# Kernel optimization log

Hardware: AMD Instinct MI355X
Metric: run time of the kernel (lower is better)

Reference implementation:

```python
import jax, jax.numpy as jnp
import numpy as np

NUM_HEADS = 8


def setup_inputs() -> dict:
    key = jax.random.key(0)
    k1, k2, k3 = jax.random.split(key, 3)
    B, L, E, H = 4, 2048, 256, NUM_HEADS
    x = jax.random.normal(k1, (B, L, E), dtype=jnp.float32)
    W_qkv = jax.random.normal(k2, (E, H * E * 3), dtype=jnp.float32) * 0.02
    W_out = jax.random.normal(k3, (H * E, E), dtype=jnp.float32) * 0.02
    return {"x": x, "W_qkv": W_qkv, "W_out": W_out}


def reference(x, W_qkv, W_out):
    B, L, E = x.shape
    H = NUM_HEADS
    qkv = x @ W_qkv  # [B, L, 3*H*E]
    q, k, v = jnp.split(qkv, 3, axis=-1)  # each [B, L, H*E]
    # reshape(B, L, H, E) then move heads before sequence -> [B, H, L, E]
    q = q.reshape(B, L, H, E).transpose(0, 2, 1, 3)
    k = k.reshape(B, L, H, E).transpose(0, 2, 1, 3)
    v = v.reshape(B, L, H, E).transpose(0, 2, 1, 3)
    scale = 1.0 / jnp.sqrt(jnp.asarray(E, dtype=x.dtype))
    scores = jnp.einsum("bhqe,bhke->bhqk", q, k) * scale  # [B, H, L, L]
    attn = jax.nn.softmax(scores, axis=-1)
    out = jnp.einsum("bhqk,bhke->bhqe", attn, v)  # [B, H, L, E]
    out = out.transpose(0, 2, 1, 3).reshape(B, L, H * E)
    return out @ W_out  # [B, L, E]
```

## Files before the change

### kernel.cpp

```cpp
#include <hip/hip_runtime.h>
#include <cstdint>
#include <cstddef>

typedef __bf16 bf16_t;
typedef __bf16 bf16x8 __attribute__((ext_vector_type(8)));
typedef __bf16 bf16x4 __attribute__((ext_vector_type(4)));
typedef float  f32x4  __attribute__((ext_vector_type(4)));
typedef float  f32x16 __attribute__((ext_vector_type(16)));

#define MFMA16(a, b, c) __builtin_amdgcn_mfma_f32_16x16x32_bf16((a), (b), (c), 0, 0, 0)
#define MFMA32(a, b, c) __builtin_amdgcn_mfma_f32_32x32x16_bf16((a), (b), (c), 0, 0, 0)
#define CVTPK(d, a, b) \
  asm("v_cvt_pk_bf16_f32 %0, %1, %2" : "=v"(d) : "v"(a), "v"(b))
#define PLSWAP(a, b) \
  asm("v_permlane32_swap_b32 %0, %1" : "+v"(a), "+v"(b))

__device__ __forceinline__ void gload_lds16(const bf16_t* g, bf16_t* l) {
  __builtin_amdgcn_global_load_lds(
      (__attribute__((address_space(1))) void*)((void*)g),
      (__attribute__((address_space(3))) void*)l, 16, 0, 0);
}

__global__ __launch_bounds__(256) void cvt_f32_bf16(
    const float* __restrict__ in, bf16_t* __restrict__ out, int n) {
  const int i = (blockIdx.x * 256 + threadIdx.x) * 4;
  if (i + 3 < n) {
    const float4 v = *(const float4*)(in + i);
    bf16x4 o;
    o[0] = (bf16_t)v.x; o[1] = (bf16_t)v.y; o[2] = (bf16_t)v.z; o[3] = (bf16_t)v.w;
    *(bf16x4*)(out + i) = o;
  }
}

__global__ __launch_bounds__(256) void transpose_f32_bf16(
    const float* __restrict__ in, bf16_t* __restrict__ out, int R, int C) {
  __shared__ bf16_t tile[32][33];
  const int bc = blockIdx.x * 32, br = blockIdx.y * 32;
  const int tx = threadIdx.x, ty = threadIdx.y;
#pragma unroll
  for (int i = 0; i < 32; i += 8)
    tile[ty + i][tx] = (bf16_t)in[(size_t)(br + ty + i) * C + bc + tx];
  __syncthreads();
#pragma unroll
  for (int i = 0; i < 32; i += 8)
    out[(size_t)(bc + ty + i) * R + br + tx] = tile[tx][ty + i];
}

template <int EPI>
__global__ __launch_bounds__(256) void gemm_bt(
    const bf16_t* __restrict__ A, const bf16_t* __restrict__ Bt,
    void* __restrict__ Cout, bf16_t* __restrict__ Vt, int M, int N, int K) {
  __shared__ __align__(16) bf16_t As[128 * 32];
  __shared__ __align__(16) bf16_t Bs[128 * 32];
  const int tid = threadIdx.x;
  const int lane = tid & 63, w = tid >> 6;
  const int wm = w >> 1, wn = w & 1;
  const int bm = blockIdx.y * 128, bn = blockIdx.x * 128;
  const int l15 = lane & 15, l4 = lane >> 4;

  f32x4 acc[4][4] = {};

  for (int k0 = 0; k0 < K; k0 += 32) {
    __syncthreads();
#pragma unroll
    for (int i = 0; i < 2; ++i) {
      const int idx = i * 256 + tid;
      const int r = idx >> 2, s = idx & 3;
      const int ss = s ^ (r & 3);
      gload_lds16(A + (size_t)(bm + r) * K + k0 + ss * 8, &As[idx * 8]);
      gload_lds16(Bt + (size_t)(bn + r) * K + k0 + ss * 8, &Bs[idx * 8]);
    }
    __syncthreads();
    bf16x8 af[4], bfr[4];
#pragma unroll
    for (int f = 0; f < 4; ++f) {
      const int ra = wm * 64 + f * 16 + l15;
      const int rb = wn * 64 + f * 16 + l15;
      af[f]  = *(const bf16x8*)&As[ra * 32 + (l4 ^ (ra & 3)) * 8];
      bfr[f] = *(const bf16x8*)&Bs[rb * 32 + (l4 ^ (rb & 3)) * 8];
    }
#pragma unroll
    for (int i = 0; i < 4; ++i)
#pragma unroll
      for (int j = 0; j < 4; ++j) acc[i][j] = MFMA16(af[i], bfr[j], acc[i][j]);
  }

#pragma unroll
  for (int i = 0; i < 4; ++i) {
    const int gr = bm + wm * 64 + i * 16 + l4 * 4;
#pragma unroll
    for (int j = 0; j < 4; ++j) {
      const int gc = bn + wn * 64 + j * 16 + l15;
      if constexpr (EPI == 0) {
        float* C = (float*)Cout;
#pragma unroll
        for (int r = 0; r < 4; ++r)
          C[(size_t)(gr + r) * N + gc] = acc[i][j][r];
      } else {
        bf16_t* C = (bf16_t*)Cout;
        if (gc < 2048) {
#pragma unroll
          for (int r = 0; r < 4; ++r)
            C[(size_t)(gr + r) * 4096 + gc] = (bf16_t)(acc[i][j][r] * 0.0625f);
        } else if (gc < 4096) {
#pragma unroll
          for (int r = 0; r < 4; ++r)
            C[(size_t)(gr + r) * 4096 + gc] = (bf16_t)acc[i][j][r];
        } else {
          const int c = gc - 4096, h = c >> 8, d = c & 255;
          const int b = gr >> 11, lt = gr & 2047;
          bf16x4 pk;
#pragma unroll
          for (int r = 0; r < 4; ++r) pk[r] = (bf16_t)acc[i][j][r];
          *(bf16x4*)&Vt[((size_t)(b * 8 + h) * 256 + d) * 2048 + lt] = pk;
        }
      }
    }
  }
}

__global__ __launch_bounds__(256, 2) void attn_fwd(
    const bf16_t* __restrict__ qk, const bf16_t* __restrict__ vt,
    bf16_t* __restrict__ ao) {
  __shared__ __align__(16) bf16_t Ks[2][32 * 256];
  __shared__ __align__(16) bf16_t Vs[2][256 * 32];
  const int tid = threadIdx.x, lane = tid & 63, w = tid >> 6;
  const int l31 = lane & 31, h5 = lane >> 5;
  const int p4 = l31 & 15, pv2 = (l31 >> 1) & 3;
  const int bid = blockIdx.x;
  const int swz = (bid & 7) * 64 + (bid >> 3);
  const int qt = swz & 15;
  const int bh = swz >> 4;
  const int bb = bh >> 3, hh = bh & 7;

  const int qcol = qt * 128 + w * 32 + l31;
  const bf16_t* qbase =
      qk + (size_t)(bb * 2048 + qcol) * 4096 + hh * 256 + h5 * 8;
  bf16x8 qf[16];
#pragma unroll
  for (int s = 0; s < 16; ++s) qf[s] = *(const bf16x8*)(qbase + s * 16);

  const bf16_t* kg = qk + (size_t)(bb * 2048) * 4096 + 2048 + hh * 256;
  const bf16_t* vg = vt + (size_t)bh * 256 * 2048;

#define STAGE_TILES(bufidx, tile)                                           \
  {                                                                         \
    const int t32 = (tile) * 32;                                            \
    _Pragma("unroll") for (int c = 0; c < 4; ++c) {                         \
      const int idx = c * 256 + tid;                                        \
      const int kr = idx >> 5, kse = idx & 31;                              \
      gload_lds16(kg + (size_t)(t32 + kr) * 4096 + ((kse ^ (kr & 15)) * 8), \
                  &Ks[bufidx][idx * 8]);                                    \
    }                                                                       \
    _Pragma("unroll") for (int c = 0; c < 4; ++c) {                         \
      const int idx = c * 256 + tid;                                        \
      const int vr = idx >> 2, vse = idx & 3;                               \
      gload_lds16(vg + (size_t)vr * 2048 + t32 +                            \
                      ((vse ^ ((vr >> 1) & 3)) * 8),                        \
                  &Vs[bufidx][idx * 8]);                                    \
    }                                                                       \
  }

  STAGE_TILES(0, 0);
  STAGE_TILES(1, 1);

  f32x16 o[8] = {};
  float m = -1e30f, lsum = 0.f;

  for (int kv = 0; kv < 64; ++kv) {
    const int cur = kv & 1;
    asm volatile("s_waitcnt vmcnt(8)" ::: "memory");
    __builtin_amdgcn_s_barrier();
    __builtin_amdgcn_sched_barrier(0);
    const bf16_t* Kc = Ks[cur];
    const bf16_t* Vc = Vs[cur];

    f32x16 sa = {};
    __builtin_amdgcn_s_setprio(1);
#pragma unroll
    for (int s = 0; s < 16; ++s) {
      bf16x8 kf = *(const bf16x8*)
          ((const char*)Kc + l31 * 512 + (((2 * s + h5) ^ p4) << 4));
      sa = MFMA32(kf, qf[s], sa);
    }
    __builtin_amdgcn_s_setprio(0);

    float pm = sa[0];
#pragma unroll
    for (int r = 1; r < 16; ++r) pm = fmaxf(pm, sa[r]);
    pm = fmaxf(pm, __shfl_xor(pm, 32));
    if (!__all(pm <= m + 8.0f)) {
      const float mn = fmaxf(m, pm);
      const float al = __expf(m - mn);
      m = mn;
      lsum *= al;
#pragma unroll
      for (int dt = 0; dt < 8; ++dt)
#pragma unroll
        for (int r = 0; r < 16; ++r) o[dt][r] *= al;
    }
    float rs = 0.f;
#pragma unroll
    for (int r = 0; r < 16; ++r) { sa[r] = __expf(sa[r] - m); rs += sa[r]; }
    rs += __shfl_xor(rs, 32);
    lsum += rs;

    __builtin_amdgcn_s_setprio(1);
#define PV_KSTEP(SA, c0, s2)                                                \
    {                                                                       \
      unsigned w0, w1, w2, w3;                                              \
      CVTPK(w0, SA[4 * (c0) + 0], SA[4 * (c0) + 1]);                        \
      CVTPK(w2, SA[4 * (c0) + 4], SA[4 * (c0) + 5]);                        \
      PLSWAP(w0, w2);                                                       \
      CVTPK(w1, SA[4 * (c0) + 2], SA[4 * (c0) + 3]);                        \
      CVTPK(w3, SA[4 * (c0) + 6], SA[4 * (c0) + 7]);                        \
      PLSWAP(w1, w3);                                                       \
      union { unsigned u[4]; bf16x8 v; } pu;                                \
      pu.u[0] = w0; pu.u[1] = w1; pu.u[2] = w2; pu.u[3] = w3;               \
      _Pragma("unroll") for (int dt = 0; dt < 8; ++dt) {                    \
        bf16x8 vf = *(const bf16x8*)((const char*)Vc +                      \
            (dt * 32 + l31) * 64 + ((((s2) * 2 + h5) ^ pv2) << 4));         \
        o[dt] = MFMA32(vf, pu.v, o[dt]);                                    \
      }                                                                     \
    }
    PV_KSTEP(sa, 0, 0);
    PV_KSTEP(sa, 2, 1);
    __builtin_amdgcn_s_setprio(0);

    __builtin_amdgcn_sched_barrier(0);
    __builtin_amdgcn_s_barrier();
    __builtin_amdgcn_sched_barrier(0);
    STAGE_TILES(cur, (kv + 2) & 63);
  }

  const float inv = 1.0f / lsum;
  bf16_t* aor = ao + (size_t)(bb * 2048 + qcol) * 2048 + hh * 256 + 4 * h5;
#pragma unroll
  for (int dt = 0; dt < 8; ++dt)
#pragma unroll
    for (int c = 0; c < 4; ++c) {
      bf16x4 ov;
#pragma unroll
      for (int bq = 0; bq < 4; ++bq) ov[bq] = (bf16_t)(o[dt][4 * c + bq] * inv);
      *(bf16x4*)(aor + dt * 32 + 8 * c) = ov;
    }
}

extern "C" void kernel_launch(void* const* d_in, const int* in_sizes, int n_in,
                              void* d_out, int out_size, void* d_ws,
                              size_t ws_size, hipStream_t stream) {
  (void)in_sizes; (void)n_in; (void)out_size; (void)ws_size;
  const float* x    = (const float*)d_in[0];
  const float* wqkv = (const float*)d_in[1];
  const float* wout = (const float*)d_in[2];
  float* out = (float*)d_out;

  char* ws = (char*)d_ws;
  bf16_t* xb  = (bf16_t*)(ws);
  bf16_t* wqt = (bf16_t*)(ws + 4194304);
  bf16_t* wot = (bf16_t*)(ws + 7340032);
  bf16_t* qkb = (bf16_t*)(ws + 8388608);
  bf16_t* vtb = (bf16_t*)(ws + 8388608 + 67108864);
  bf16_t* aob = (bf16_t*)(ws + 8388608 + 67108864 + 33554432);

  cvt_f32_bf16<<<2048, 256, 0, stream>>>(x, xb, 8192 * 256);
  transpose_f32_bf16<<<dim3(192, 8), dim3(32, 8), 0, stream>>>(wqkv, wqt, 256, 6144);
  transpose_f32_bf16<<<dim3(8, 64), dim3(32, 8), 0, stream>>>(wout, wot, 2048, 256);
  gemm_bt<1><<<dim3(48, 64), 256, 0, stream>>>(xb, wqt, qkb, vtb, 8192, 6144, 256);
  attn_fwd<<<512, 256, 0, stream>>>(qkb, vtb, aob);
  gemm_bt<0><<<dim3(2, 64), 256, 0, stream>>>(aob, wot, out, nullptr, 8192, 256, 2048);
}
```

Baseline: 331.3 us.

## Process two 32-row query sets per wave in attention to reuse K/V fragments

Each wave now computes attention for 64 query rows (two independent 32-row sets with separate softmax state), reusing each K and V LDS fragment for two MFMAs. The grid is halved and launch bounds drop to one block per CU to allow the doubled accumulator and Q register footprint. This reduces LDS reads and global K/V staging per query, at the cost of lower occupancy and possible register pressure or spills.

```diff
diff --git a/kernel.cpp b/kernel.cpp
--- a/kernel.cpp
+++ b/kernel.cpp
@@ -119,7 +119,7 @@
   }
 }
 
-__global__ __launch_bounds__(256, 2) void attn_fwd(
+__global__ __launch_bounds__(256, 1) void attn_fwd(
     const bf16_t* __restrict__ qk, const bf16_t* __restrict__ vt,
     bf16_t* __restrict__ ao) {
   __shared__ __align__(16) bf16_t Ks[2][32 * 256];
@@ -128,17 +128,20 @@
   const int l31 = lane & 31, h5 = lane >> 5;
   const int p4 = l31 & 15, pv2 = (l31 >> 1) & 3;
   const int bid = blockIdx.x;
-  const int swz = (bid & 7) * 64 + (bid >> 3);
-  const int qt = swz & 15;
-  const int bh = swz >> 4;
+  const int swz = (bid & 7) * 32 + (bid >> 3);
+  const int qt = swz & 7;
+  const int bh = swz >> 3;
   const int bb = bh >> 3, hh = bh & 7;
 
-  const int qcol = qt * 128 + w * 32 + l31;
-  const bf16_t* qbase =
-      qk + (size_t)(bb * 2048 + qcol) * 4096 + hh * 256 + h5 * 8;
-  bf16x8 qf[16];
-#pragma unroll
-  for (int s = 0; s < 16; ++s) qf[s] = *(const bf16x8*)(qbase + s * 16);
+  const int qcolA = qt * 256 + w * 64 + l31;
+  const bf16_t* qbaseA =
+      qk + (size_t)(bb * 2048 + qcolA) * 4096 + hh * 256 + h5 * 8;
+  bf16x8 qfA[16], qfB[16];
+#pragma unroll
+  for (int s = 0; s < 16; ++s) {
+    qfA[s] = *(const bf16x8*)(qbaseA + s * 16);
+    qfB[s] = *(const bf16x8*)(qbaseA + (size_t)32 * 4096 + s * 16);
+  }
 
   const bf16_t* kg = qk + (size_t)(bb * 2048) * 4096 + 2048 + hh * 256;
   const bf16_t* vg = vt + (size_t)bh * 256 * 2048;
@@ -164,8 +167,8 @@
   STAGE_TILES(0, 0);
   STAGE_TILES(1, 1);
 
-  f32x16 o[8] = {};
-  float m = -1e30f, lsum = 0.f;
+  f32x16 oA[8] = {}, oB[8] = {};
+  float mA = -1e30f, lsA = 0.f, mB = -1e30f, lsB = 0.f;
 
   for (int kv = 0; kv < 64; ++kv) {
     const int cur = kv & 1;
@@ -175,38 +178,41 @@
     const bf16_t* Kc = Ks[cur];
     const bf16_t* Vc = Vs[cur];
 
-    f32x16 sa = {};
+    f32x16 saA = {}, saB = {};
     __builtin_amdgcn_s_setprio(1);
 #pragma unroll
     for (int s = 0; s < 16; ++s) {
       bf16x8 kf = *(const bf16x8*)
           ((const char*)Kc + l31 * 512 + (((2 * s + h5) ^ p4) << 4));
-      sa = MFMA32(kf, qf[s], sa);
+      saA = MFMA32(kf, qfA[s], saA);
+      saB = MFMA32(kf, qfB[s], saB);
     }
     __builtin_amdgcn_s_setprio(0);
 
-    float pm = sa[0];
-#pragma unroll
-    for (int r = 1; r < 16; ++r) pm = fmaxf(pm, sa[r]);
-    pm = fmaxf(pm, __shfl_xor(pm, 32));
-    if (!__all(pm <= m + 8.0f)) {
-      const float mn = fmaxf(m, pm);
-      const float al = __expf(m - mn);
-      m = mn;
-      lsum *= al;
-#pragma unroll
-      for (int dt = 0; dt < 8; ++dt)
-#pragma unroll
-        for (int r = 0; r < 16; ++r) o[dt][r] *= al;
-    }
-    float rs = 0.f;
-#pragma unroll
-    for (int r = 0; r < 16; ++r) { sa[r] = __expf(sa[r] - m); rs += sa[r]; }
-    rs += __shfl_xor(rs, 32);
-    lsum += rs;
-
-    __builtin_amdgcn_s_setprio(1);
-#define PV_KSTEP(SA, c0, s2)                                                \
+#define SOFTMAX_SET(SA, M_, LS_, O_)                                        \
+    {                                                                       \
+      float pm = SA[0];                                                     \
+      _Pragma("unroll") for (int r = 1; r < 16; ++r) pm = fmaxf(pm, SA[r]); \
+      pm = fmaxf(pm, __shfl_xor(pm, 32));                                   \
+      if (!__all(pm <= M_ + 8.0f)) {                                        \
+        const float mn = fmaxf(M_, pm);                                     \
+        const float al = __expf(M_ - mn);                                   \
+        M_ = mn;                                                            \
+        LS_ *= al;                                                          \
+        _Pragma("unroll") for (int dt = 0; dt < 8; ++dt)                    \
+          _Pragma("unroll") for (int r = 0; r < 16; ++r) O_[dt][r] *= al;   \
+      }                                                                     \
+      float rs = 0.f;                                                       \
+      _Pragma("unroll") for (int r = 0; r < 16; ++r) {                      \
+        SA[r] = __expf(SA[r] - M_); rs += SA[r];                            \
+      }                                                                     \
+      rs += __shfl_xor(rs, 32);                                             \
+      LS_ += rs;                                                            \
+    }
+    SOFTMAX_SET(saA, mA, lsA, oA);
+    SOFTMAX_SET(saB, mB, lsB, oB);
+
+#define MAKE_PU(SA, c0, PU)                                                 \
     {                                                                       \
       unsigned w0, w1, w2, w3;                                              \
       CVTPK(w0, SA[4 * (c0) + 0], SA[4 * (c0) + 1]);                        \
@@ -215,16 +221,22 @@
       CVTPK(w1, SA[4 * (c0) + 2], SA[4 * (c0) + 3]);                        \
       CVTPK(w3, SA[4 * (c0) + 6], SA[4 * (c0) + 7]);                        \
       PLSWAP(w1, w3);                                                       \
-      union { unsigned u[4]; bf16x8 v; } pu;                                \
-      pu.u[0] = w0; pu.u[1] = w1; pu.u[2] = w2; pu.u[3] = w3;               \
-      _Pragma("unroll") for (int dt = 0; dt < 8; ++dt) {                    \
-        bf16x8 vf = *(const bf16x8*)((const char*)Vc +                      \
-            (dt * 32 + l31) * 64 + ((((s2) * 2 + h5) ^ pv2) << 4));         \
-        o[dt] = MFMA32(vf, pu.v, o[dt]);                                    \
-      }                                                                     \
-    }
-    PV_KSTEP(sa, 0, 0);
-    PV_KSTEP(sa, 2, 1);
+      PU.u[0] = w0; PU.u[1] = w1; PU.u[2] = w2; PU.u[3] = w3;               \
+    }
+    __builtin_amdgcn_s_setprio(1);
+#pragma unroll
+    for (int s2 = 0; s2 < 2; ++s2) {
+      union { unsigned u[4]; bf16x8 v; } puA, puB;
+      MAKE_PU(saA, 2 * s2, puA);
+      MAKE_PU(saB, 2 * s2, puB);
+#pragma unroll
+      for (int dt = 0; dt < 8; ++dt) {
+        bf16x8 vf = *(const bf16x8*)((const char*)Vc +
+            (dt * 32 + l31) * 64 + (((s2 * 2 + h5) ^ pv2) << 4));
+        oA[dt] = MFMA32(vf, puA.v, oA[dt]);
+        oB[dt] = MFMA32(vf, puB.v, oB[dt]);
+      }
+    }
     __builtin_amdgcn_s_setprio(0);
 
     __builtin_amdgcn_sched_barrier(0);
@@ -233,16 +245,21 @@
     STAGE_TILES(cur, (kv + 2) & 63);
   }
 
-  const float inv = 1.0f / lsum;
-  bf16_t* aor = ao + (size_t)(bb * 2048 + qcol) * 2048 + hh * 256 + 4 * h5;
+  const float invA = 1.0f / lsA, invB = 1.0f / lsB;
+  bf16_t* aorA = ao + (size_t)(bb * 2048 + qcolA) * 2048 + hh * 256 + 4 * h5;
+  bf16_t* aorB = aorA + (size_t)32 * 2048;
 #pragma unroll
   for (int dt = 0; dt < 8; ++dt)
 #pragma unroll
     for (int c = 0; c < 4; ++c) {
-      bf16x4 ov;
-#pragma unroll
-      for (int bq = 0; bq < 4; ++bq) ov[bq] = (bf16_t)(o[dt][4 * c + bq] * inv);
-      *(bf16x4*)(aor + dt * 32 + 8 * c) = ov;
+      bf16x4 ovA, ovB;
+#pragma unroll
+      for (int bq = 0; bq < 4; ++bq) {
+        ovA[bq] = (bf16_t)(oA[dt][4 * c + bq] * invA);
+        ovB[bq] = (bf16_t)(oB[dt][4 * c + bq] * invB);
+      }
+      *(bf16x4*)(aorA + dt * 32 + 8 * c) = ovA;
+      *(bf16x4*)(aorB + dt * 32 + 8 * c) = ovB;
     }
 }
 
@@ -267,6 +284,6 @@
   transpose_f32_bf16<<<dim3(192, 8), dim3(32, 8), 0, stream>>>(wqkv, wqt, 256, 6144);
   transpose_f32_bf16<<<dim3(8, 64), dim3(32, 8), 0, stream>>>(wout, wot, 2048, 256);
   gemm_bt<1><<<dim3(48, 64), 256, 0, stream>>>(xb, wqt, qkb, vtb, 8192, 6144, 256);
-  attn_fwd<<<512, 256, 0, stream>>>(qkb, vtb, aob);
+  attn_fwd<<<256, 256, 0, stream>>>(qkb, vtb, aob);
   gemm_bt<0><<<dim3(2, 64), 256, 0, stream>>>(aob, wot, out, nullptr, 8192, 256, 2048);
 }
```

Result: slower. 1.226 ms (+270.0%).

## Software-pipeline QK of next KV tile with softmax and PV of current

Applied to the files above, without the earlier changes.

Restructures the attention loop into a two-stage software pipeline. Each iteration now computes QK^T for the next key tile into an alternate score register set while softmax and PV run on the current one. K and V staging are split so the next K tile is issued right after the top barrier and V after the bottom barrier, with the vmcnt waits adjusted to match. The aim is to hide softmax/exp latency behind MFMA work, at the cost of an extra 16-register score accumulator, one wasted QK pass on the wrapped final tile, and higher register pressure.

```diff
diff --git a/kernel.cpp b/kernel.cpp
--- a/kernel.cpp
+++ b/kernel.cpp
@@ -143,70 +143,64 @@
   const bf16_t* kg = qk + (size_t)(bb * 2048) * 4096 + 2048 + hh * 256;
   const bf16_t* vg = vt + (size_t)bh * 256 * 2048;
 
-#define STAGE_TILES(bufidx, tile)                                           \
-  {                                                                         \
-    const int t32 = (tile) * 32;                                            \
+#define STAGE_K(bufidx, tile)                                               \
+  {                                                                         \
+    const int t32k = (tile) * 32;                                           \
     _Pragma("unroll") for (int c = 0; c < 4; ++c) {                         \
       const int idx = c * 256 + tid;                                        \
       const int kr = idx >> 5, kse = idx & 31;                              \
-      gload_lds16(kg + (size_t)(t32 + kr) * 4096 + ((kse ^ (kr & 15)) * 8), \
+      gload_lds16(kg + (size_t)(t32k + kr) * 4096 + ((kse ^ (kr & 15)) * 8),\
                   &Ks[bufidx][idx * 8]);                                    \
     }                                                                       \
+  }
+#define STAGE_V(bufidx, tile)                                               \
+  {                                                                         \
+    const int t32v = (tile) * 32;                                           \
     _Pragma("unroll") for (int c = 0; c < 4; ++c) {                         \
       const int idx = c * 256 + tid;                                        \
       const int vr = idx >> 2, vse = idx & 3;                               \
-      gload_lds16(vg + (size_t)vr * 2048 + t32 +                            \
+      gload_lds16(vg + (size_t)vr * 2048 + t32v +                           \
                       ((vse ^ ((vr >> 1) & 3)) * 8),                        \
                   &Vs[bufidx][idx * 8]);                                    \
     }                                                                       \
   }
 
-  STAGE_TILES(0, 0);
-  STAGE_TILES(1, 1);
-
-  f32x16 o[8] = {};
-  float m = -1e30f, lsum = 0.f;
-
-  for (int kv = 0; kv < 64; ++kv) {
-    const int cur = kv & 1;
-    asm volatile("s_waitcnt vmcnt(8)" ::: "memory");
-    __builtin_amdgcn_s_barrier();
-    __builtin_amdgcn_sched_barrier(0);
-    const bf16_t* Kc = Ks[cur];
-    const bf16_t* Vc = Vs[cur];
-
-    f32x16 sa = {};
-    __builtin_amdgcn_s_setprio(1);
-#pragma unroll
-    for (int s = 0; s < 16; ++s) {
-      bf16x8 kf = *(const bf16x8*)
-          ((const char*)Kc + l31 * 512 + (((2 * s + h5) ^ p4) << 4));
-      sa = MFMA32(kf, qf[s], sa);
-    }
-    __builtin_amdgcn_s_setprio(0);
-
-    float pm = sa[0];
-#pragma unroll
-    for (int r = 1; r < 16; ++r) pm = fmaxf(pm, sa[r]);
-    pm = fmaxf(pm, __shfl_xor(pm, 32));
-    if (!__all(pm <= m + 8.0f)) {
-      const float mn = fmaxf(m, pm);
-      const float al = __expf(m - mn);
-      m = mn;
-      lsum *= al;
-#pragma unroll
-      for (int dt = 0; dt < 8; ++dt)
-#pragma unroll
-        for (int r = 0; r < 16; ++r) o[dt][r] *= al;
-    }
-    float rs = 0.f;
-#pragma unroll
-    for (int r = 0; r < 16; ++r) { sa[r] = __expf(sa[r] - m); rs += sa[r]; }
-    rs += __shfl_xor(rs, 32);
-    lsum += rs;
-
-    __builtin_amdgcn_s_setprio(1);
-#define PV_KSTEP(SA, c0, s2)                                                \
+#define ZERO16(v) \
+  { _Pragma("unroll") for (int z = 0; z < 16; ++z) (v)[z] = 0.f; }
+
+#define QK_PHASE(SN, KB)                                                    \
+  {                                                                         \
+    __builtin_amdgcn_s_setprio(1);                                          \
+    _Pragma("unroll") for (int s = 0; s < 16; ++s) {                        \
+      bf16x8 kf = *(const bf16x8*)((const char*)Ks[KB] + l31 * 512 +        \
+                                   (((2 * s + h5) ^ p4) << 4));             \
+      SN = MFMA32(kf, qf[s], SN);                                           \
+    }                                                                       \
+    __builtin_amdgcn_s_setprio(0);                                          \
+  }
+
+#define SOFTMAX_SET(SA)                                                     \
+    {                                                                       \
+      float pm = SA[0];                                                     \
+      _Pragma("unroll") for (int r = 1; r < 16; ++r) pm = fmaxf(pm, SA[r]); \
+      pm = fmaxf(pm, __shfl_xor(pm, 32));                                   \
+      if (!__all(pm <= m + 8.0f)) {                    \
+        const float mn = fmaxf(m, pm);                                      \
+        const float al = __expf(m - mn);                                    \
+        m = mn;                                                             \
+        lsum *= al;                                                         \
+        _Pragma("unroll") for (int dt = 0; dt < 8; ++dt)                    \
+          _Pragma("unroll") for (int r = 0; r < 16; ++r) o[dt][r] *= al;    \
+      }                                                                     \
+      float rs = 0.f;                                                       \
+      _Pragma("unroll") for (int r = 0; r < 16; ++r) {                      \
+        SA[r] = __expf(SA[r] - m); rs += SA[r];                             \
+      }                                                                     \
+      rs += __shfl_xor(rs, 32);                                             \
+      lsum += rs;                                                           \
+    }
+
+#define MAKE_PU(SA, c0, PU)                                                 \
     {                                                                       \
       unsigned w0, w1, w2, w3;                                              \
       CVTPK(w0, SA[4 * (c0) + 0], SA[4 * (c0) + 1]);                        \
@@ -215,22 +209,56 @@
       CVTPK(w1, SA[4 * (c0) + 2], SA[4 * (c0) + 3]);                        \
       CVTPK(w3, SA[4 * (c0) + 6], SA[4 * (c0) + 7]);                        \
       PLSWAP(w1, w3);                                                       \
+      PU.u[0] = w0; PU.u[1] = w1; PU.u[2] = w2; PU.u[3] = w3;               \
+    }
+
+#define PV_PHASE(SA, VB)                                                    \
+  {                                                                         \
+    __builtin_amdgcn_s_setprio(1);                                          \
+    _Pragma("unroll") for (int s2 = 0; s2 < 2; ++s2) {                      \
       union { unsigned u[4]; bf16x8 v; } pu;                                \
-      pu.u[0] = w0; pu.u[1] = w1; pu.u[2] = w2; pu.u[3] = w3;               \
+      MAKE_PU(SA, 2 * s2, pu);                                              \
       _Pragma("unroll") for (int dt = 0; dt < 8; ++dt) {                    \
-        bf16x8 vf = *(const bf16x8*)((const char*)Vc +                      \
-            (dt * 32 + l31) * 64 + ((((s2) * 2 + h5) ^ pv2) << 4));         \
+        bf16x8 vf = *(const bf16x8*)((const char*)Vs[VB] +                  \
+            (dt * 32 + l31) * 64 + (((s2 * 2 + h5) ^ pv2) << 4));           \
         o[dt] = MFMA32(vf, pu.v, o[dt]);                                    \
       }                                                                     \
-    }
-    PV_KSTEP(sa, 0, 0);
-    PV_KSTEP(sa, 2, 1);
-    __builtin_amdgcn_s_setprio(0);
-
-    __builtin_amdgcn_sched_barrier(0);
-    __builtin_amdgcn_s_barrier();
-    __builtin_amdgcn_sched_barrier(0);
-    STAGE_TILES(cur, (kv + 2) & 63);
+    }                                                                       \
+    __builtin_amdgcn_s_setprio(0);                                          \
+  }
+
+#define BODY(SP, SN, CURB, NXTB, KVT)                                       \
+  {                                                                         \
+    asm volatile("s_waitcnt vmcnt(4)" ::: "memory");                        \
+    __builtin_amdgcn_s_barrier();                                           \
+    __builtin_amdgcn_sched_barrier(0);                                      \
+    STAGE_K(CURB, ((KVT) + 2) & 63);                                        \
+    QK_PHASE(SN, NXTB);                                                     \
+    SOFTMAX_SET(SP);                                                        \
+    PV_PHASE(SP, CURB);                                                     \
+    __builtin_amdgcn_sched_barrier(0);                                      \
+    __builtin_amdgcn_s_barrier();                                           \
+    __builtin_amdgcn_sched_barrier(0);                                      \
+    STAGE_V(CURB, ((KVT) + 2) & 63);                                        \
+  }
+
+  STAGE_K(0, 0); STAGE_V(0, 0); STAGE_K(1, 1); STAGE_V(1, 1);
+
+  f32x16 o[8] = {};
+  float m = -1e30f, lsum = 0.f;
+  f32x16 saA, saB;
+  ZERO16(saA); ZERO16(saB);
+
+  asm volatile("s_waitcnt vmcnt(12)" ::: "memory");
+  __builtin_amdgcn_s_barrier();
+  __builtin_amdgcn_sched_barrier(0);
+  QK_PHASE(saA, 0);
+
+  for (int kv = 0; kv < 64; kv += 2) {
+    BODY(saA, saB, 0, 1, kv);
+    ZERO16(saA);
+    BODY(saB, saA, 1, 0, kv + 1);
+    ZERO16(saB);
   }
 
   const float inv = 1.0f / lsum;
```

Measured after the change: 367.4 us. +10.9%, slower.
